# Optimization experiments

Measured on AMD Instinct MI355X. Metric: run time of the kernel, lower is better.

The kernel has to match this reference:

```python
import jax, jax.numpy as jnp
import numpy as np

B, S, D, H = 4, 2048, 1024, 16
HD = D // H  # head dim = 64


def setup_inputs() -> dict:
    key = jax.random.key(0)
    ks = jax.random.split(key, 11)
    std = 1.0 / np.sqrt(D)
    return {
        "query": jax.random.normal(ks[0], (B, S, D), jnp.float32),
        "key": jax.random.normal(ks[1], (B, S, D), jnp.float32),
        "value": jax.random.normal(ks[2], (B, S, D), jnp.float32),
        "Wq": jax.random.normal(ks[3], (D, D), jnp.float32) * std,
        "bq": jnp.zeros((D,), jnp.float32),
        "Wk": jax.random.normal(ks[4], (D, D), jnp.float32) * std,
        "bk": jnp.zeros((D,), jnp.float32),
        "Wv": jax.random.normal(ks[5], (D, D), jnp.float32) * std,
        "bv": jnp.zeros((D,), jnp.float32),
        "Wo": jax.random.normal(ks[6], (D, D), jnp.float32) * std,
        "bo": jnp.zeros((D,), jnp.float32),
    }


def reference(query, key, value, Wq, bq, Wk, bk, Wv, bv, Wo, bo):
    scale = jnp.sqrt(jnp.float32(D))  # NOTE: module scales by sqrt(hid_dim), not sqrt(head_dim)
    # nn.Linear: x @ W.T + b
    def split_heads(x):
        return x.reshape(B, -1, H, HD).transpose(0, 2, 1, 3)  # [B,H,S,HD]
    Q = split_heads(query @ Wq.T + bq)
    K = split_heads(key @ Wk.T + bk)
    V = split_heads(value @ Wv.T + bv)
    energy = jnp.einsum("bhqd,bhkd->bhqk", Q, K) / scale  # [B,H,S,S]
    attention = jax.nn.softmax(energy, axis=-1)  # dropout is identity in eval / p=0
    X = jnp.einsum("bhqk,bhkd->bhqd", attention, V)  # [B,H,S,HD]
    X = X.transpose(0, 2, 1, 3).reshape(B, -1, D)  # [B,S,D]
    return X @ Wo.T + bo
```

## Files before the change

kernel.cpp:

```cpp
#include <hip/hip_runtime.h>
#include <stdint.h>

#define DEVI __device__ __forceinline__

typedef __attribute__((ext_vector_type(8))) __bf16 bf16x8;
typedef __attribute__((ext_vector_type(4))) __bf16 bf16x4;
typedef __attribute__((ext_vector_type(4))) float f32x4;
typedef __attribute__((ext_vector_type(4))) unsigned short u16x4;
typedef __attribute__((ext_vector_type(4))) unsigned int u32x4;
typedef unsigned short u16;

constexpr int Bn = 4, Sn = 2048, Dn = 1024, Hn = 16;
constexpr int Mn = Bn * Sn;
constexpr float QSCALE = 1.4426950408889634f / 32.0f;
constexpr float SSHIFT = -16.0f;

DEVI u16 f2bf(float f) {
  uint32_t u = __builtin_bit_cast(uint32_t, f);
  u += 0x7fffu + ((u >> 16) & 1u);
  return (u16)(u >> 16);
}

typedef __attribute__((address_space(1))) void gvoid;
typedef __attribute__((address_space(3))) void lvoid;
DEVI void gload_lds16(const void* g, void* l) {
  __builtin_amdgcn_global_load_lds((gvoid*)(uintptr_t)g,
                                   (lvoid*)(uint32_t)(uintptr_t)l, 16, 0, 0);
}

DEVI f32x4 mfma16(bf16x8 a, bf16x8 b, f32x4 c) {
  return __builtin_amdgcn_mfma_f32_16x16x32_bf16(a, b, c, 0, 0, 0);
}

struct CastArgs {
  const float* src[7];
  u16* dst[7];
  int n[7];
};

__global__ __launch_bounds__(256) void cast_kernel(CastArgs a) {
  const int seg = blockIdx.y;
  const float* __restrict__ src = a.src[seg];
  u16* __restrict__ dst = a.dst[seg];
  const int n = a.n[seg];
  const int stride = gridDim.x * 256 * 4;
  for (int i = (blockIdx.x * 256 + threadIdx.x) * 4; i < n; i += stride) {
    const float4 v = *reinterpret_cast<const float4*>(src + i);
    u16x4 p;
    p[0] = f2bf(v.x); p[1] = f2bf(v.y); p[2] = f2bf(v.z); p[3] = f2bf(v.w);
    *reinterpret_cast<u16x4*>(dst + i) = p;
  }
}


#define GEMM_PRE(Aptr, Btptr)                                                 \
  const int tid = threadIdx.x, lane = tid & 63, w = tid >> 6;                 \
  const int wr = w >> 2, wc = w & 3;                                          \
  const int c = lane & 15, g = lane >> 4;                                     \
  const int srow = tid >> 2;                                                  \
  const int scolb = ((tid & 3) * 16) ^ ((srow & 3) << 4);                     \
  const u16* aSrc  = (Aptr)  + (size_t)(m0 + srow) * 1024 + (scolb >> 1);     \
  const u16* bSrc0 = (Btptr) + (size_t)(n0 + srow) * 1024 + (scolb >> 1);     \
  const u16* bSrc1 = (Btptr) + (size_t)(n0 + 128 + srow) * 1024 + (scolb >> 1); \
  const int ldsOff = w * 1024;                                                \
  const int aB = (wr * 64 + c) * 64 + ((g * 16) ^ ((c & 3) << 4));            \
  const int bB = (wc * 64 + c) * 64 + ((g * 16) ^ ((c & 3) << 4));

#define GSTAGE(BUF, KT_)                                                      \
  {                                                                           \
    gload_lds16(aSrc + (KT_), (char*)As[BUF] + ldsOff);                       \
    gload_lds16(bSrc0 + (KT_), (char*)Bs[BUF] + ldsOff);                      \
    gload_lds16(bSrc1 + (KT_), (char*)Bs[BUF] + 8192 + ldsOff);               \
  }

#define GTILE(BUF, SBUF, KT)                                                  \
  {                                                                           \
    asm volatile("s_waitcnt vmcnt(3)" ::: "memory");                          \
    __builtin_amdgcn_sched_barrier(0);                                        \
    __builtin_amdgcn_s_barrier();                                             \
    __builtin_amdgcn_sched_barrier(0);                                        \
    GSTAGE(SBUF, ((KT) + 64) & 1023);                                         \
    bf16x8 af[4], bfq[4];                                                     \
    _Pragma("unroll")                                                         \
    for (int i = 0; i < 4; ++i)                                               \
      af[i] = *(const bf16x8*)((const char*)As[BUF] + aB + i * 1024);         \
    _Pragma("unroll")                                                         \
    for (int i = 0; i < 4; ++i)                                               \
      bfq[i] = *(const bf16x8*)((const char*)Bs[BUF] + bB + i * 1024);        \
    __builtin_amdgcn_s_setprio(1);                                            \
    _Pragma("unroll")                                                         \
    for (int mi = 0; mi < 4; ++mi)                                            \
      _Pragma("unroll")                                                       \
      for (int ni = 0; ni < 4; ++ni)                                          \
        acc[mi][ni] = mfma16(af[mi], bfq[ni], acc[mi][ni]);                   \
    __builtin_amdgcn_s_setprio(0);                                            \
  }

#define GEMM_LOOP                                                             \
  GSTAGE(0, 0);                                                               \
  GSTAGE(1, 32);                                                              \
  for (int kt = 0; kt < 960; kt += 96) {                                      \
    GTILE(0, 2, kt);                                                          \
    GTILE(1, 0, kt + 32);                                                     \
    GTILE(2, 1, kt + 64);                                                     \
  }                                                                           \
  GTILE(0, 2, 960);                                                           \
  GTILE(1, 0, 992);

struct QKVArgs {
  const u16 *Aq, *Ak, *Av, *Wq, *Wk, *Wv;
  const float *bq, *bk, *bv;
  u16 *Qh, *Kh, *Vt;
};

__global__ __launch_bounds__(512, 4)
void qkv_gemm(QKVArgs a) {
  __shared__ __align__(16) u16 As[3][128 * 32];
  __shared__ __align__(16) u16 Bs[3][256 * 32];

  const int raw = blockIdx.x;
  const int swz = (raw & 7) * 96 + (raw >> 3);
  const int which = swz >> 8;
  const int bid = swz & 255;
  const u16* __restrict__ A  = which == 0 ? a.Aq : which == 1 ? a.Ak : a.Av;
  const u16* __restrict__ Bt = which == 0 ? a.Wq : which == 1 ? a.Wk : a.Wv;
  const float* __restrict__ bias = which == 0 ? a.bq : which == 1 ? a.bk : a.bv;

  const int mt = bid >> 2, nt = bid & 3;
  const int m0 = mt * 128, n0 = nt * 256;

  GEMM_PRE(A, Bt)
  f32x4 acc[4][4] = {};
  GEMM_LOOP

  #pragma unroll
  for (int mi = 0; mi < 4; ++mi) {
    #pragma unroll
    for (int ni = 0; ni < 4; ++ni) {
      const int n = n0 + wc * 64 + ni * 16 + c;
      const float bv = bias[n];
      const int mb = m0 + wr * 64 + mi * 16 + g * 4;
      const f32x4 v = acc[mi][ni];
      const int h = n >> 6, hd = n & 63;
      if (which == 2) {
        const int b = mb >> 11, s = mb & 2047;
        u16x4 pk;
        #pragma unroll
        for (int j = 0; j < 4; ++j) pk[j] = f2bf(v[j] + bv);
        *(u16x4*)(a.Vt + ((size_t)((b * Hn + h) * 64 + hd)) * Sn + s) = pk;
      } else {
        u16* dst = which == 0 ? a.Qh : a.Kh;
        const float sc = which == 0 ? QSCALE : 1.0f;
        #pragma unroll
        for (int j = 0; j < 4; ++j) {
          const int m = mb + j;
          const int b = m >> 11, s = m & 2047;
          dst[(((size_t)(b * Hn + h) * Sn + s) << 6) + hd] = f2bf((v[j] + bv) * sc);
        }
      }
    }
  }
}

__global__ __launch_bounds__(512, 4)
void gemm_out(const u16* __restrict__ A, const u16* __restrict__ Bt,
              const float* __restrict__ bias, float* __restrict__ out) {
  __shared__ __align__(16) u16 As[3][128 * 32];
  __shared__ __align__(16) u16 Bs[3][256 * 32];

  const int raw = blockIdx.x;
  const int swz = (raw & 7) * 32 + (raw >> 3);
  const int mt = swz >> 2, nt = swz & 3;
  const int m0 = mt * 128, n0 = nt * 256;

  GEMM_PRE(A, Bt)
  f32x4 acc[4][4] = {};
  GEMM_LOOP

  #pragma unroll
  for (int mi = 0; mi < 4; ++mi) {
    #pragma unroll
    for (int ni = 0; ni < 4; ++ni) {
      const int n = n0 + wc * 64 + ni * 16 + c;
      const float bv = bias[n];
      const int mb = m0 + wr * 64 + mi * 16 + g * 4;
      const f32x4 v = acc[mi][ni];
      #pragma unroll
      for (int j = 0; j < 4; ++j)
        out[(size_t)(mb + j) * Dn + n] = v[j] + bv;
    }
  }
}

#undef GEMM_LOOP
#undef GTILE
#undef GSTAGE
#undef GEMM_PRE

__global__ __launch_bounds__(512, 4)
void flash_attn(const u16* __restrict__ Q, const u16* __restrict__ K,
                const u16* __restrict__ Vt, u16* __restrict__ X) {
  __shared__ __align__(16) u16 Ks[3][4096];
  __shared__ __align__(16) u16 Vs[3][4096];

  const int tid = threadIdx.x, lane = tid & 63, w = tid >> 6;
  const int bid = blockIdx.x;
  const int bh = bid & 63, qt = bid >> 6;
  const int b = bh >> 4, h = bh & 15;
  const int q0 = qt * 128 + w * 16;
  const int c = lane & 15, g = lane >> 4;

  const u16* Qb = Q + (size_t)bh * Sn * 64;
  const u16* Kb = K + (size_t)bh * Sn * 64;
  const u16* Vb = Vt + (size_t)bh * 64 * Sn;

  const int srow = tid >> 3;
  const int scol = (((tid & 7) * 16) ^ ((srow & 7) << 4)) >> 1;
  const int srcK = srow * 64 + scol;
  const int srcV = srow * Sn + scol;
  const int ldsOff = w * 1024;
#define STAGE(BUF, KV_)                                                   \
  {                                                                       \
    gload_lds16(Kb + (size_t)(KV_) * 64 + srcK, (char*)Ks[BUF] + ldsOff); \
    gload_lds16(Vb + (KV_) + srcV, (char*)Vs[BUF] + ldsOff);              \
  }

  const int laneB0 = c * 128 + ((g * 16) ^ ((c & 7) << 4));
  const int laneB1 = c * 128 + ((64 + g * 16) ^ ((c & 7) << 4));

  bf16x8 qf[2];
  #pragma unroll
  for (int ks = 0; ks < 2; ++ks)
    qf[ks] = *(const bf16x8*)(Qb + (size_t)(q0 + c) * 64 + ks * 32 + g * 8);

  bf16x8 ONES;
  #pragma unroll
  for (int e = 0; e < 8; ++e) ONES[e] = (__bf16)1.0f;
  const f32x4 SINITv = {SSHIFT, SSHIFT, SSHIFT, SSHIFT};

  STAGE(0, 0);
  STAGE(1, 64);

  f32x4 o[4] = {};
  f32x4 lacc = {};

#define TILE(BUF, SBUF, KV)                                                   \
  {                                                                           \
    asm volatile("s_waitcnt vmcnt(2)" ::: "memory");                          \
    __builtin_amdgcn_sched_barrier(0);                                        \
    __builtin_amdgcn_s_barrier();                                             \
    __builtin_amdgcn_sched_barrier(0);                                        \
    STAGE(SBUF, ((KV) + 128) & (Sn - 1));                                     \
    f32x4 sc[4];                                                              \
    {                                                                         \
      bf16x8 kfr[4];                                                          \
      _Pragma("unroll")                                                       \
      for (int kf = 0; kf < 4; ++kf)                                          \
        kfr[kf] = *(const bf16x8*)((const char*)Ks[BUF] + laneB0 + kf * 2048);\
      __builtin_amdgcn_s_setprio(1);                                          \
      _Pragma("unroll")                                                       \
      for (int kf = 0; kf < 4; ++kf)                                          \
        sc[kf] = mfma16(kfr[kf], qf[0], SINITv);                              \
      __builtin_amdgcn_s_setprio(0);                                          \
      _Pragma("unroll")                                                       \
      for (int kf = 0; kf < 4; ++kf)                                          \
        kfr[kf] = *(const bf16x8*)((const char*)Ks[BUF] + laneB1 + kf * 2048);\
      __builtin_amdgcn_s_setprio(1);                                          \
      _Pragma("unroll")                                                       \
      for (int kf = 0; kf < 4; ++kf)                                          \
        sc[kf] = mfma16(kfr[kf], qf[1], sc[kf]);                              \
      __builtin_amdgcn_s_setprio(0);                                          \
    }                                                                         \
    uint32_t wvv[4][2];                                                       \
    _Pragma("unroll")                                                         \
    for (int kf = 0; kf < 4; ++kf) {                                          \
      const float p0 = __builtin_exp2f(sc[kf][0]);                            \
      const float p1 = __builtin_exp2f(sc[kf][1]);                            \
      const float p2 = __builtin_exp2f(sc[kf][2]);                            \
      const float p3 = __builtin_exp2f(sc[kf][3]);                            \
      asm("v_cvt_pk_bf16_f32 %0, %1, %2" : "=v"(wvv[kf][0]) : "v"(p0), "v"(p1)); \
      asm("v_cvt_pk_bf16_f32 %0, %1, %2" : "=v"(wvv[kf][1]) : "v"(p2), "v"(p3)); \
    }                                                                         \
    bf16x8 pa[2];                                                             \
    _Pragma("unroll")                                                         \
    for (int ks2 = 0; ks2 < 2; ++ks2) {                                       \
      uint32_t ua = wvv[2 * ks2][0], ub = wvv[2 * ks2][1];                    \
      uint32_t uc = wvv[2 * ks2 + 1][0], ud = wvv[2 * ks2 + 1][1];            \
      asm("v_permlane32_swap_b32 %0, %1" : "+v"(ua), "+v"(uc));               \
      asm("v_permlane32_swap_b32 %0, %1" : "+v"(ub), "+v"(ud));               \
      asm("v_permlane16_swap_b32 %0, %1" : "+v"(ua), "+v"(uc));               \
      asm("v_permlane16_swap_b32 %0, %1" : "+v"(ub), "+v"(ud));               \
      const u32x4 uv = {ua, ub, uc, ud};                                      \
      pa[ks2] = __builtin_bit_cast(bf16x8, uv);                               \
    }                                                                         \
    lacc = mfma16(pa[0], ONES, lacc);                                         \
    lacc = mfma16(pa[1], ONES, lacc);                                         \
    {                                                                         \
      bf16x8 vfr[4];                                                          \
      _Pragma("unroll")                                                       \
      for (int nd = 0; nd < 4; ++nd)                                          \
        vfr[nd] = *(const bf16x8*)((const char*)Vs[BUF] + laneB0 + nd * 2048);\
      __builtin_amdgcn_s_setprio(1);                                          \
      _Pragma("unroll")                                                       \
      for (int nd = 0; nd < 4; ++nd)                                          \
        o[nd] = mfma16(pa[0], vfr[nd], o[nd]);                                \
      __builtin_amdgcn_s_setprio(0);                                          \
      _Pragma("unroll")                                                       \
      for (int nd = 0; nd < 4; ++nd)                                          \
        vfr[nd] = *(const bf16x8*)((const char*)Vs[BUF] + laneB1 + nd * 2048);\
      __builtin_amdgcn_s_setprio(1);                                          \
      _Pragma("unroll")                                                       \
      for (int nd = 0; nd < 4; ++nd)                                          \
        o[nd] = mfma16(pa[1], vfr[nd], o[nd]);                                \
      __builtin_amdgcn_s_setprio(0);                                          \
    }                                                                         \
  }

  for (int kv = 0; kv < 1920; kv += 192) {
    TILE(0, 2, kv);
    TILE(1, 0, kv + 64);
    TILE(2, 1, kv + 128);
  }
  TILE(0, 2, 1920);
  TILE(1, 0, 1984);
#undef TILE
#undef STAGE

  #pragma unroll
  for (int j = 0; j < 4; ++j) {
    const float rn = 1.0f / lacc[j];
    const int s = q0 + g * 4 + j;
    u16* dst = X + (size_t)(b * Sn + s) * Dn + h * 64 + c;
    #pragma unroll
    for (int nd = 0; nd < 4; ++nd)
      dst[nd * 16] = f2bf(o[nd][j] * rn);
  }
}

extern "C" void kernel_launch(void* const* d_in, const int* in_sizes, int n_in,
                              void* d_out, int out_size, void* d_ws, size_t ws_size,
                              hipStream_t stream) {
  (void)in_sizes; (void)n_in; (void)out_size; (void)ws_size;
  const float* query = (const float*)d_in[0];
  const float* key_  = (const float*)d_in[1];
  const float* value = (const float*)d_in[2];
  const float* Wq = (const float*)d_in[3];
  const float* bq = (const float*)d_in[4];
  const float* Wk = (const float*)d_in[5];
  const float* bk = (const float*)d_in[6];
  const float* Wv = (const float*)d_in[7];
  const float* bv = (const float*)d_in[8];
  const float* Wo = (const float*)d_in[9];
  const float* bo = (const float*)d_in[10];

  char* ws = (char*)d_ws;
  size_t off = 0;
  auto alloc = [&](size_t bytes) {
    void* p = ws + off;
    off += (bytes + 255) & ~(size_t)255;
    return p;
  };
  const size_t actB = (size_t)Mn * Dn * 2;
  const size_t wB = (size_t)Dn * Dn * 2;
  u16* qbuf = (u16*)alloc(actB);
  u16* kbuf = (u16*)alloc(actB);
  u16* vbuf = (u16*)alloc(actB);
  u16* wqb = (u16*)alloc(wB);
  u16* wkb = (u16*)alloc(wB);
  u16* wvb = (u16*)alloc(wB);
  u16* wob = (u16*)alloc(wB);
  u16* Qh = (u16*)alloc(actB);
  u16* Kh = (u16*)alloc(actB);
  u16* Vt = (u16*)alloc(actB);
  u16* Xb = qbuf;

  CastArgs ca;
  ca.src[0] = query; ca.src[1] = key_; ca.src[2] = value;
  ca.src[3] = Wq; ca.src[4] = Wk; ca.src[5] = Wv; ca.src[6] = Wo;
  ca.dst[0] = qbuf; ca.dst[1] = kbuf; ca.dst[2] = vbuf;
  ca.dst[3] = wqb; ca.dst[4] = wkb; ca.dst[5] = wvb; ca.dst[6] = wob;
  ca.n[0] = ca.n[1] = ca.n[2] = Mn * Dn;
  ca.n[3] = ca.n[4] = ca.n[5] = ca.n[6] = Dn * Dn;
  cast_kernel<<<dim3(1024, 7), 256, 0, stream>>>(ca);

  QKVArgs qa;
  qa.Aq = qbuf; qa.Ak = kbuf; qa.Av = vbuf;
  qa.Wq = wqb; qa.Wk = wkb; qa.Wv = wvb;
  qa.bq = bq; qa.bk = bk; qa.bv = bv;
  qa.Qh = Qh; qa.Kh = Kh; qa.Vt = Vt;
  qkv_gemm<<<dim3(768), 512, 0, stream>>>(qa);

  flash_attn<<<dim3(Bn * Hn * (Sn / 128)), 512, 0, stream>>>(Qh, Kh, Vt, Xb);
  gemm_out<<<dim3(256), 512, 0, stream>>>(Xb, wob, bo, (float*)d_out);
}
```

Measured before the change: 216.7 us.

## Fuse fp32-to-bf16 activation cast into QKV GEMM A-tile loading

Stops pre-casting the three fp32 activation tensors in a separate pass. The QKV GEMM now loads fp32 A rows through registers, converts them with packed bf16 conversion instructions, and writes them to a double-buffered LDS tile, while B still streams via direct global-to-LDS loads. This removes a full extra read and write of the activations. In exchange, A loads now pass through VGPRs and the LDS stores add an lgkmcnt wait and extra register pressure inside the pipelined loop.

After: 230.3 us. 6.3% more time.

```diff
diff --git a/kernel.cpp b/kernel.cpp
--- a/kernel.cpp
+++ b/kernel.cpp
@@ -33,9 +33,9 @@
 }
 
 struct CastArgs {
-  const float* src[7];
-  u16* dst[7];
-  int n[7];
+  const float* src[4];
+  u16* dst[4];
+  int n[4];
 };
 
 __global__ __launch_bounds__(256) void cast_kernel(CastArgs a) {
@@ -52,86 +52,110 @@
   }
 }
 
-
-#define GEMM_PRE(Aptr, Btptr)                                                 \
-  const int tid = threadIdx.x, lane = tid & 63, w = tid >> 6;                 \
-  const int wr = w >> 2, wc = w & 3;                                          \
-  const int c = lane & 15, g = lane >> 4;                                     \
-  const int srow = tid >> 2;                                                  \
-  const int scolb = ((tid & 3) * 16) ^ ((srow & 3) << 4);                     \
-  const u16* aSrc  = (Aptr)  + (size_t)(m0 + srow) * 1024 + (scolb >> 1);     \
-  const u16* bSrc0 = (Btptr) + (size_t)(n0 + srow) * 1024 + (scolb >> 1);     \
-  const u16* bSrc1 = (Btptr) + (size_t)(n0 + 128 + srow) * 1024 + (scolb >> 1); \
-  const int ldsOff = w * 1024;                                                \
-  const int aB = (wr * 64 + c) * 64 + ((g * 16) ^ ((c & 3) << 4));            \
-  const int bB = (wc * 64 + c) * 64 + ((g * 16) ^ ((c & 3) << 4));
-
-#define GSTAGE(BUF, KT_)                                                      \
-  {                                                                           \
-    gload_lds16(aSrc + (KT_), (char*)As[BUF] + ldsOff);                       \
-    gload_lds16(bSrc0 + (KT_), (char*)Bs[BUF] + ldsOff);                      \
-    gload_lds16(bSrc1 + (KT_), (char*)Bs[BUF] + 8192 + ldsOff);               \
-  }
-
-#define GTILE(BUF, SBUF, KT)                                                  \
-  {                                                                           \
-    asm volatile("s_waitcnt vmcnt(3)" ::: "memory");                          \
-    __builtin_amdgcn_sched_barrier(0);                                        \
-    __builtin_amdgcn_s_barrier();                                             \
-    __builtin_amdgcn_sched_barrier(0);                                        \
-    GSTAGE(SBUF, ((KT) + 64) & 1023);                                         \
-    bf16x8 af[4], bfq[4];                                                     \
-    _Pragma("unroll")                                                         \
-    for (int i = 0; i < 4; ++i)                                               \
-      af[i] = *(const bf16x8*)((const char*)As[BUF] + aB + i * 1024);         \
-    _Pragma("unroll")                                                         \
-    for (int i = 0; i < 4; ++i)                                               \
-      bfq[i] = *(const bf16x8*)((const char*)Bs[BUF] + bB + i * 1024);        \
-    __builtin_amdgcn_s_setprio(1);                                            \
-    _Pragma("unroll")                                                         \
-    for (int mi = 0; mi < 4; ++mi)                                            \
-      _Pragma("unroll")                                                       \
-      for (int ni = 0; ni < 4; ++ni)                                          \
-        acc[mi][ni] = mfma16(af[mi], bfq[ni], acc[mi][ni]);                   \
-    __builtin_amdgcn_s_setprio(0);                                            \
-  }
-
-#define GEMM_LOOP                                                             \
-  GSTAGE(0, 0);                                                               \
-  GSTAGE(1, 32);                                                              \
-  for (int kt = 0; kt < 960; kt += 96) {                                      \
-    GTILE(0, 2, kt);                                                          \
-    GTILE(1, 0, kt + 32);                                                     \
-    GTILE(2, 1, kt + 64);                                                     \
-  }                                                                           \
-  GTILE(0, 2, 960);                                                           \
-  GTILE(1, 0, 992);
-
 struct QKVArgs {
-  const u16 *Aq, *Ak, *Av, *Wq, *Wk, *Wv;
+  const float *Aq, *Ak, *Av;
+  const u16 *Wq, *Wk, *Wv;
   const float *bq, *bk, *bv;
   u16 *Qh, *Kh, *Vt;
 };
 
 __global__ __launch_bounds__(512, 4)
 void qkv_gemm(QKVArgs a) {
-  __shared__ __align__(16) u16 As[3][128 * 32];
+  __shared__ __align__(16) u16 As[2][128 * 32];
   __shared__ __align__(16) u16 Bs[3][256 * 32];
 
   const int raw = blockIdx.x;
   const int swz = (raw & 7) * 96 + (raw >> 3);
   const int which = swz >> 8;
   const int bid = swz & 255;
-  const u16* __restrict__ A  = which == 0 ? a.Aq : which == 1 ? a.Ak : a.Av;
-  const u16* __restrict__ Bt = which == 0 ? a.Wq : which == 1 ? a.Wk : a.Wv;
+  const float* __restrict__ A = which == 0 ? a.Aq : which == 1 ? a.Ak : a.Av;
+  const u16* __restrict__ Bt  = which == 0 ? a.Wq : which == 1 ? a.Wk : a.Wv;
   const float* __restrict__ bias = which == 0 ? a.bq : which == 1 ? a.bk : a.bv;
 
   const int mt = bid >> 2, nt = bid & 3;
   const int m0 = mt * 128, n0 = nt * 256;
 
-  GEMM_PRE(A, Bt)
+  const int tid = threadIdx.x, lane = tid & 63, w = tid >> 6;
+  const int wr = w >> 2, wc = w & 3;
+  const int c = lane & 15, g = lane >> 4;
+  const int srow = tid >> 2;
+  const int scolb = ((tid & 3) * 16) ^ ((srow & 3) << 4);
+  const float* aSrc = A + (size_t)(m0 + srow) * 1024 + (tid & 3) * 8;
+  const u16* bSrc0 = Bt + (size_t)(n0 + srow) * 1024 + (scolb >> 1);
+  const u16* bSrc1 = Bt + (size_t)(n0 + 128 + srow) * 1024 + (scolb >> 1);
+  const int ldsOff = w * 1024;
+  const int aDst = srow * 64 + (((tid & 3) * 16) ^ ((srow & 3) << 4));
+  const int aB = (wr * 64 + c) * 64 + ((g * 16) ^ ((c & 3) << 4));
+  const int bB = (wc * 64 + c) * 64 + ((g * 16) ^ ((c & 3) << 4));
+
   f32x4 acc[4][4] = {};
-  GEMM_LOOP
+
+#define QSTAGE_B(BUF, KT_)                                                    \
+  {                                                                           \
+    gload_lds16(bSrc0 + (KT_), (char*)Bs[BUF] + ldsOff);                      \
+    gload_lds16(bSrc1 + (KT_), (char*)Bs[BUF] + 8192 + ldsOff);               \
+  }
+
+#define QA_CVT_WRITE(WBUF, A0, A1)                                            \
+  {                                                                           \
+    uint32_t w0_, w1_, w2_, w3_;                                              \
+    asm("v_cvt_pk_bf16_f32 %0, %1, %2" : "=v"(w0_) : "v"((A0).x), "v"((A0).y)); \
+    asm("v_cvt_pk_bf16_f32 %0, %1, %2" : "=v"(w1_) : "v"((A0).z), "v"((A0).w)); \
+    asm("v_cvt_pk_bf16_f32 %0, %1, %2" : "=v"(w2_) : "v"((A1).x), "v"((A1).y)); \
+    asm("v_cvt_pk_bf16_f32 %0, %1, %2" : "=v"(w3_) : "v"((A1).z), "v"((A1).w)); \
+    const u32x4 uv_ = {w0_, w1_, w2_, w3_};                                   \
+    *(u32x4*)((char*)As[WBUF] + aDst) = uv_;                                  \
+  }
+
+#define QTILE(BUFA, WBUFA, BUFB, SBUFB, KT)                                   \
+  {                                                                           \
+    asm volatile("s_waitcnt lgkmcnt(0)" ::: "memory");                        \
+    __builtin_amdgcn_sched_barrier(0);                                        \
+    __builtin_amdgcn_s_barrier();                                             \
+    __builtin_amdgcn_sched_barrier(0);                                        \
+    const float4 a0_ = *(const float4*)(aSrc + (((KT) + 32) & 1023));         \
+    const float4 a1_ = *(const float4*)(aSrc + (((KT) + 32) & 1023) + 4);     \
+    QSTAGE_B(SBUFB, ((KT) + 64) & 1023);                                      \
+    __builtin_amdgcn_sched_barrier(0);                                        \
+    bf16x8 af[4], bfq[4];                                                     \
+    _Pragma("unroll")                                                         \
+    for (int i = 0; i < 4; ++i)                                               \
+      af[i] = *(const bf16x8*)((const char*)As[BUFA] + aB + i * 1024);        \
+    _Pragma("unroll")                                                         \
+    for (int i = 0; i < 4; ++i)                                               \
+      bfq[i] = *(const bf16x8*)((const char*)Bs[BUFB] + bB + i * 1024);       \
+    __builtin_amdgcn_s_setprio(1);                                            \
+    _Pragma("unroll")                                                         \
+    for (int mi = 0; mi < 4; ++mi)                                            \
+      _Pragma("unroll")                                                       \
+      for (int ni = 0; ni < 4; ++ni)                                          \
+        acc[mi][ni] = mfma16(af[mi], bfq[ni], acc[mi][ni]);                   \
+    __builtin_amdgcn_s_setprio(0);                                            \
+    __builtin_amdgcn_sched_barrier(0);                                        \
+    QA_CVT_WRITE(WBUFA, a0_, a1_);                                            \
+  }
+
+  QSTAGE_B(0, 0);
+  QSTAGE_B(1, 32);
+  {
+    const float4 a0_ = *(const float4*)(aSrc);
+    const float4 a1_ = *(const float4*)(aSrc + 4);
+    QA_CVT_WRITE(0, a0_, a1_);
+  }
+
+  for (int kt = 0; kt < 960; kt += 192) {
+    QTILE(0, 1, 0, 2, kt);
+    QTILE(1, 0, 1, 0, kt + 32);
+    QTILE(0, 1, 2, 1, kt + 64);
+    QTILE(1, 0, 0, 2, kt + 96);
+    QTILE(0, 1, 1, 0, kt + 128);
+    QTILE(1, 0, 2, 1, kt + 160);
+  }
+  QTILE(0, 1, 0, 2, 960);
+  QTILE(1, 0, 1, 0, 992);
+#undef QTILE
+#undef QA_CVT_WRITE
+#undef QSTAGE_B
 
   #pragma unroll
   for (int mi = 0; mi < 4; ++mi) {
@@ -173,9 +197,61 @@
   const int mt = swz >> 2, nt = swz & 3;
   const int m0 = mt * 128, n0 = nt * 256;
 
-  GEMM_PRE(A, Bt)
+  const int tid = threadIdx.x, lane = tid & 63, w = tid >> 6;
+  const int wr = w >> 2, wc = w & 3;
+  const int c = lane & 15, g = lane >> 4;
+  const int srow = tid >> 2;
+  const int scolb = ((tid & 3) * 16) ^ ((srow & 3) << 4);
+  const u16* aSrc  = A  + (size_t)(m0 + srow) * 1024 + (scolb >> 1);
+  const u16* bSrc0 = Bt + (size_t)(n0 + srow) * 1024 + (scolb >> 1);
+  const u16* bSrc1 = Bt + (size_t)(n0 + 128 + srow) * 1024 + (scolb >> 1);
+  const int ldsOff = w * 1024;
+  const int aB = (wr * 64 + c) * 64 + ((g * 16) ^ ((c & 3) << 4));
+  const int bB = (wc * 64 + c) * 64 + ((g * 16) ^ ((c & 3) << 4));
+
   f32x4 acc[4][4] = {};
-  GEMM_LOOP
+
+#define OSTAGE(BUF, KT_)                                                      \
+  {                                                                           \
+    gload_lds16(aSrc + (KT_), (char*)As[BUF] + ldsOff);                       \
+    gload_lds16(bSrc0 + (KT_), (char*)Bs[BUF] + ldsOff);                      \
+    gload_lds16(bSrc1 + (KT_), (char*)Bs[BUF] + 8192 + ldsOff);               \
+  }
+
+#define OTILE(BUF, SBUF, KT)                                                  \
+  {                                                                           \
+    asm volatile("s_waitcnt vmcnt(3)" ::: "memory");                          \
+    __builtin_amdgcn_sched_barrier(0);                                        \
+    __builtin_amdgcn_s_barrier();                                             \
+    __builtin_amdgcn_sched_barrier(0);                                        \
+    OSTAGE(SBUF, ((KT) + 64) & 1023);                                         \
+    bf16x8 af[4], bfq[4];                                                     \
+    _Pragma("unroll")                                                         \
+    for (int i = 0; i < 4; ++i)                                               \
+      af[i] = *(const bf16x8*)((const char*)As[BUF] + aB + i * 1024);         \
+    _Pragma("unroll")                                                         \
+    for (int i = 0; i < 4; ++i)                                               \
+      bfq[i] = *(const bf16x8*)((const char*)Bs[BUF] + bB + i * 1024);        \
+    __builtin_amdgcn_s_setprio(1);                                            \
+    _Pragma("unroll")                                                         \
+    for (int mi = 0; mi < 4; ++mi)                                            \
+      _Pragma("unroll")                                                       \
+      for (int ni = 0; ni < 4; ++ni)                                          \
+        acc[mi][ni] = mfma16(af[mi], bfq[ni], acc[mi][ni]);                   \
+    __builtin_amdgcn_s_setprio(0);                                            \
+  }
+
+  OSTAGE(0, 0);
+  OSTAGE(1, 32);
+  for (int kt = 0; kt < 960; kt += 96) {
+    OTILE(0, 2, kt);
+    OTILE(1, 0, kt + 32);
+    OTILE(2, 1, kt + 64);
+  }
+  OTILE(0, 2, 960);
+  OTILE(1, 0, 992);
+#undef OTILE
+#undef OSTAGE
 
   #pragma unroll
   for (int mi = 0; mi < 4; ++mi) {
@@ -191,11 +267,6 @@
     }
   }
 }
-
-#undef GEMM_LOOP
-#undef GTILE
-#undef GSTAGE
-#undef GEMM_PRE
 
 __global__ __launch_bounds__(512, 4)
 void flash_attn(const u16* __restrict__ Q, const u16* __restrict__ K,
@@ -362,9 +433,6 @@
   };
   const size_t actB = (size_t)Mn * Dn * 2;
   const size_t wB = (size_t)Dn * Dn * 2;
-  u16* qbuf = (u16*)alloc(actB);
-  u16* kbuf = (u16*)alloc(actB);
-  u16* vbuf = (u16*)alloc(actB);
   u16* wqb = (u16*)alloc(wB);
   u16* wkb = (u16*)alloc(wB);
   u16* wvb = (u16*)alloc(wB);
@@ -372,19 +440,16 @@
   u16* Qh = (u16*)alloc(actB);
   u16* Kh = (u16*)alloc(actB);
   u16* Vt = (u16*)alloc(actB);
-  u16* Xb = qbuf;
+  u16* Xb = (u16*)alloc(actB);
 
   CastArgs ca;
-  ca.src[0] = query; ca.src[1] = key_; ca.src[2] = value;
-  ca.src[3] = Wq; ca.src[4] = Wk; ca.src[5] = Wv; ca.src[6] = Wo;
-  ca.dst[0] = qbuf; ca.dst[1] = kbuf; ca.dst[2] = vbuf;
-  ca.dst[3] = wqb; ca.dst[4] = wkb; ca.dst[5] = wvb; ca.dst[6] = wob;
-  ca.n[0] = ca.n[1] = ca.n[2] = Mn * Dn;
-  ca.n[3] = ca.n[4] = ca.n[5] = ca.n[6] = Dn * Dn;
-  cast_kernel<<<dim3(1024, 7), 256, 0, stream>>>(ca);
+  ca.src[0] = Wq; ca.src[1] = Wk; ca.src[2] = Wv; ca.src[3] = Wo;
+  ca.dst[0] = wqb; ca.dst[1] = wkb; ca.dst[2] = wvb; ca.dst[3] = wob;
+  ca.n[0] = ca.n[1] = ca.n[2] = ca.n[3] = Dn * Dn;
+  cast_kernel<<<dim3(1024, 4), 256, 0, stream>>>(ca);
 
   QKVArgs qa;
-  qa.Aq = qbuf; qa.Ak = kbuf; qa.Av = vbuf;
+  qa.Aq = query; qa.Ak = key_; qa.Av = value;
   qa.Wq = wqb; qa.Wk = wkb; qa.Wv = wvb;
   qa.bq = bq; qa.bk = bk; qa.bv = bv;
   qa.Qh = Qh; qa.Kh = Kh; qa.Vt = Vt;
```

## Software-pipeline attention so the next tile's QK overlaps current softmax and PV

Applied to the files above, without the earlier changes.

Splits the attention tile body into a QK block and a finalize block (exp, pack, row-sum, PV), and runs them with a one-tile skew. The scores for the next KV tile are computed while the current tile's scores are turned into probabilities and multiplied by V. Double-buffered score registers and an explicit prologue and epilogue replace the old loop, which also drops the wrapped dummy loads past the end. The cost is more live registers, which may lower occupancy. Each step now waits with vmcnt(0) instead of vmcnt(2), which shortens how far global-to-LDS prefetch runs ahead of compute.

Result: no change. 214.9 us (-0.8%).

```diff
diff --git a/kernel.cpp b/kernel.cpp
--- a/kernel.cpp
+++ b/kernel.cpp
@@ -51,7 +51,6 @@
     *reinterpret_cast<u16x4*>(dst + i) = p;
   }
 }
-
 
 #define GEMM_PRE(Aptr, Btptr)                                                 \
   const int tid = threadIdx.x, lane = tid & 63, w = tid >> 6;                 \
@@ -238,46 +237,40 @@
   for (int e = 0; e < 8; ++e) ONES[e] = (__bf16)1.0f;
   const f32x4 SINITv = {SSHIFT, SSHIFT, SSHIFT, SSHIFT};
 
-  STAGE(0, 0);
-  STAGE(1, 64);
-
   f32x4 o[4] = {};
   f32x4 lacc = {};
-
-#define TILE(BUF, SBUF, KV)                                                   \
+  f32x4 scA[4], scB[4];
+
+#define QK_BLOCK(KB, SCT)                                                     \
   {                                                                           \
-    asm volatile("s_waitcnt vmcnt(2)" ::: "memory");                          \
-    __builtin_amdgcn_sched_barrier(0);                                        \
-    __builtin_amdgcn_s_barrier();                                             \
-    __builtin_amdgcn_sched_barrier(0);                                        \
-    STAGE(SBUF, ((KV) + 128) & (Sn - 1));                                     \
-    f32x4 sc[4];                                                              \
-    {                                                                         \
-      bf16x8 kfr[4];                                                          \
-      _Pragma("unroll")                                                       \
-      for (int kf = 0; kf < 4; ++kf)                                          \
-        kfr[kf] = *(const bf16x8*)((const char*)Ks[BUF] + laneB0 + kf * 2048);\
-      __builtin_amdgcn_s_setprio(1);                                          \
-      _Pragma("unroll")                                                       \
-      for (int kf = 0; kf < 4; ++kf)                                          \
-        sc[kf] = mfma16(kfr[kf], qf[0], SINITv);                              \
-      __builtin_amdgcn_s_setprio(0);                                          \
-      _Pragma("unroll")                                                       \
-      for (int kf = 0; kf < 4; ++kf)                                          \
-        kfr[kf] = *(const bf16x8*)((const char*)Ks[BUF] + laneB1 + kf * 2048);\
-      __builtin_amdgcn_s_setprio(1);                                          \
-      _Pragma("unroll")                                                       \
-      for (int kf = 0; kf < 4; ++kf)                                          \
-        sc[kf] = mfma16(kfr[kf], qf[1], sc[kf]);                              \
-      __builtin_amdgcn_s_setprio(0);                                          \
-    }                                                                         \
+    bf16x8 kfr[4];                                                            \
+    _Pragma("unroll")                                                         \
+    for (int kf = 0; kf < 4; ++kf)                                            \
+      kfr[kf] = *(const bf16x8*)((const char*)Ks[KB] + laneB0 + kf * 2048);   \
+    __builtin_amdgcn_s_setprio(1);                                            \
+    _Pragma("unroll")                                                         \
+    for (int kf = 0; kf < 4; ++kf)                                            \
+      SCT[kf] = mfma16(kfr[kf], qf[0], SINITv);                               \
+    __builtin_amdgcn_s_setprio(0);                                            \
+    _Pragma("unroll")                                                         \
+    for (int kf = 0; kf < 4; ++kf)                                            \
+      kfr[kf] = *(const bf16x8*)((const char*)Ks[KB] + laneB1 + kf * 2048);   \
+    __builtin_amdgcn_s_setprio(1);                                            \
+    _Pragma("unroll")                                                         \
+    for (int kf = 0; kf < 4; ++kf)                                            \
+      SCT[kf] = mfma16(kfr[kf], qf[1], SCT[kf]);                              \
+    __builtin_amdgcn_s_setprio(0);                                            \
+  }
+
+#define FIN_BLOCK(VB, SCT)                                                    \
+  {                                                                           \
     uint32_t wvv[4][2];                                                       \
     _Pragma("unroll")                                                         \
     for (int kf = 0; kf < 4; ++kf) {                                          \
-      const float p0 = __builtin_exp2f(sc[kf][0]);                            \
-      const float p1 = __builtin_exp2f(sc[kf][1]);                            \
-      const float p2 = __builtin_exp2f(sc[kf][2]);                            \
-      const float p3 = __builtin_exp2f(sc[kf][3]);                            \
+      const float p0 = __builtin_exp2f(SCT[kf][0]);                           \
+      const float p1 = __builtin_exp2f(SCT[kf][1]);                           \
+      const float p2 = __builtin_exp2f(SCT[kf][2]);                           \
+      const float p3 = __builtin_exp2f(SCT[kf][3]);                           \
       asm("v_cvt_pk_bf16_f32 %0, %1, %2" : "=v"(wvv[kf][0]) : "v"(p0), "v"(p1)); \
       asm("v_cvt_pk_bf16_f32 %0, %1, %2" : "=v"(wvv[kf][1]) : "v"(p2), "v"(p3)); \
     }                                                                         \
@@ -299,7 +292,7 @@
       bf16x8 vfr[4];                                                          \
       _Pragma("unroll")                                                       \
       for (int nd = 0; nd < 4; ++nd)                                          \
-        vfr[nd] = *(const bf16x8*)((const char*)Vs[BUF] + laneB0 + nd * 2048);\
+        vfr[nd] = *(const bf16x8*)((const char*)Vs[VB] + laneB0 + nd * 2048); \
       __builtin_amdgcn_s_setprio(1);                                          \
       _Pragma("unroll")                                                       \
       for (int nd = 0; nd < 4; ++nd)                                          \
@@ -307,7 +300,7 @@
       __builtin_amdgcn_s_setprio(0);                                          \
       _Pragma("unroll")                                                       \
       for (int nd = 0; nd < 4; ++nd)                                          \
-        vfr[nd] = *(const bf16x8*)((const char*)Vs[BUF] + laneB1 + nd * 2048);\
+        vfr[nd] = *(const bf16x8*)((const char*)Vs[VB] + laneB1 + nd * 2048); \
       __builtin_amdgcn_s_setprio(1);                                          \
       _Pragma("unroll")                                                       \
       for (int nd = 0; nd < 4; ++nd)                                          \
@@ -316,14 +309,43 @@
     }                                                                         \
   }
 
-  for (int kv = 0; kv < 1920; kv += 192) {
-    TILE(0, 2, kv);
-    TILE(1, 0, kv + 64);
-    TILE(2, 1, kv + 128);
-  }
-  TILE(0, 2, 1920);
-  TILE(1, 0, 1984);
-#undef TILE
+#define PIPE(KB, VB, SB, KV, CURT, NXTT)                                      \
+  {                                                                           \
+    asm volatile("s_waitcnt vmcnt(0)" ::: "memory");                          \
+    __builtin_amdgcn_sched_barrier(0);                                        \
+    __builtin_amdgcn_s_barrier();                                             \
+    __builtin_amdgcn_sched_barrier(0);                                        \
+    STAGE(SB, (KV) + 128);                                                    \
+    QK_BLOCK(KB, NXTT);                                                       \
+    FIN_BLOCK(VB, CURT);                                                      \
+  }
+
+  STAGE(0, 0);
+  STAGE(1, 64);
+  asm volatile("s_waitcnt vmcnt(2)" ::: "memory");
+  __builtin_amdgcn_sched_barrier(0);
+  __builtin_amdgcn_s_barrier();
+  __builtin_amdgcn_sched_barrier(0);
+  QK_BLOCK(0, scA);
+
+  for (int kv = 0; kv < 1920; kv += 384) {
+    PIPE(1, 0, 2, kv,       scA, scB);
+    PIPE(2, 1, 0, kv + 64,  scB, scA);
+    PIPE(0, 2, 1, kv + 128, scA, scB);
+    PIPE(1, 0, 2, kv + 192, scB, scA);
+    PIPE(2, 1, 0, kv + 256, scA, scB);
+    PIPE(0, 2, 1, kv + 320, scB, scA);
+  }
+  asm volatile("s_waitcnt vmcnt(0)" ::: "memory");
+  __builtin_amdgcn_sched_barrier(0);
+  __builtin_amdgcn_s_barrier();
+  __builtin_amdgcn_sched_barrier(0);
+  QK_BLOCK(1, scB);
+  FIN_BLOCK(0, scA);
+  FIN_BLOCK(1, scB);
+#undef PIPE
+#undef FIN_BLOCK
+#undef QK_BLOCK
 #undef STAGE
 
   #pragma unroll
```
